# Kernel tuning notes

Measured on AMD Instinct MI355X. Metric: run time of the kernel, lower is better.

## Reference

```python
import jax, jax.numpy as jnp
import numpy as np

N = 8192
EMBED_DIM = 128
TAU = 0.2
MAX_SAMPLES = 10
NEG_INF = -1e9


def setup_inputs() -> dict:
    key = jax.random.key(0)
    k1, k2, k3, k4, k5, k6 = jax.random.split(key, 6)
    user_emb = jax.random.normal(k1, (N, EMBED_DIM), dtype=jnp.float32)
    item_emb = jax.random.normal(k2, (N, EMBED_DIM), dtype=jnp.float32)
    social_edges = jax.random.randint(k3, (2, 131072), 0, N, dtype=jnp.int64)
    # Linear(embed_dim, embed_dim) params
    lim = 1.0 / np.sqrt(EMBED_DIM)
    W = jax.random.uniform(k4, (EMBED_DIM, EMBED_DIM), minval=-lim, maxval=lim, dtype=jnp.float32)
    b = jax.random.uniform(k5, (EMBED_DIM,), minval=-lim, maxval=lim, dtype=jnp.float32)
    # gumbel noise: -log(Exp(1)) == standard Gumbel, matches -empty.exponential_().log()
    gumbel = jax.random.gumbel(k6, (N, N), dtype=jnp.float32)
    return {"user_emb": user_emb, "item_emb": item_emb, "social_edges": social_edges,
            "W": W, "b": b, "gumbel": gumbel}


def reference(user_emb, item_emb, social_edges, W, b, gumbel):
    # projection + similarity
    proj = user_emb @ W.T + b                      # [N, D]
    sim = (proj @ proj.T) / TAU                    # [N, N]
    # mask = eye + scatter of social edges
    mask = jnp.eye(N, dtype=jnp.float32)
    mask = mask.at[social_edges[0], social_edges[1]].set(1.0)
    sim = jnp.where(mask > 0, NEG_INF, sim)
    # gumbel-softmax (soft)
    y_soft = jax.nn.softmax((sim + gumbel) / TAU, axis=-1)
    # top-k scatter -> binary relation matrix
    k = min(MAX_SAMPLES, N - 1)
    _, topk_idx = jax.lax.top_k(y_soft, k)         # [N, k]
    rows = jnp.arange(N)[:, None]
    new_relations = jnp.zeros_like(sim).at[rows, topk_idx].set(1.0)
    return new_relations
```

## Files before the change

### kernel.cpp

```cpp
#include <hip/hip_runtime.h>

#define NROW 8192
#define DIM 128
#define NWORD (NROW / 32)
#define CAP 448
#define MINNORM 1.17549435082228751e-38f

__device__ __attribute__((aligned(16))) float g_Pf[(size_t)NROW * DIM];
__device__ unsigned int g_mask[(size_t)NROW * NWORD];
__device__ float g_ct[(size_t)NROW * CAP];
__device__ int   g_ci[(size_t)NROW * CAP];
__device__ int   g_cnt[NROW];
__device__ unsigned int g_umax[NROW];
__device__ int g_flag;

__device__ __forceinline__ unsigned int umap(float f) {
    unsigned int u = __float_as_uint(f);
    return (u & 0x80000000u) ? ~u : (u | 0x80000000u);
}
__device__ __forceinline__ float finv(unsigned int m) {
    if (m == 0u) return -3.4e38f;
    return (m & 0x80000000u) ? __uint_as_float(m & 0x7FFFFFFFu)
                             : __uint_as_float(~m);
}

__global__ void init_kernel() {
    int i = blockIdx.x * 256 + threadIdx.x;
    if (i < NROW * NWORD) g_mask[i] = 0u;
    if (i < NROW) { g_cnt[i] = 0; g_umax[i] = 0u; }
}

__global__ void detect_i64_kernel(const unsigned int* __restrict__ w) {
    __shared__ unsigned int s;
    if (threadIdx.x == 0) s = 0u;
    __syncthreads();
    unsigned int acc = 0u;
    for (int e = threadIdx.x; e < 4096; e += 256) acc |= w[2 * e + 1];
    atomicOr(&s, acc);
    __syncthreads();
    if (threadIdx.x == 0) g_flag = (s == 0u) ? 1 : 0;
}

__global__ void scatter_edges_kernel(const int* __restrict__ edges, int nedge) {
    int e = blockIdx.x * blockDim.x + threadIdx.x;
    if (e >= nedge) return;
    int r, c;
    if (g_flag) { r = edges[2 * e]; c = edges[2 * (nedge + e)]; }
    else        { r = edges[e];     c = edges[nedge + e]; }
    atomicOr(&g_mask[(size_t)r * NWORD + (c >> 5)], 1u << (c & 31));
}

__global__ void diag_mask_kernel() {
    int i = blockIdx.x * blockDim.x + threadIdx.x;
    atomicOr(&g_mask[(size_t)i * NWORD + (i >> 5)], 1u << (i & 31));
}

__global__ __launch_bounds__(256) void proj_kernel(const float* __restrict__ U,
                                                   const float* __restrict__ W,
                                                   const float* __restrict__ bias) {
    __shared__ float Ws[64][DIM];
    __shared__ float Ur[16][DIM];
    const int tid = threadIdx.x;
    const int i0 = blockIdx.x * 16;
    for (int idx = tid; idx < 16 * DIM; idx += 256)
        ((float*)Ur)[idx] = U[(size_t)i0 * DIM + idx];
    for (int half = 0; half < 2; ++half) {
        __syncthreads();
        for (int idx = tid; idx < 64 * DIM; idx += 256)
            ((float*)Ws)[idx] = W[(size_t)half * 64 * DIM + idx];
        __syncthreads();
        const int d = tid & 63;
        const int rg = tid >> 6;
        const float bb = bias[half * 64 + d];
#pragma unroll
        for (int rr = 0; rr < 4; ++rr) {
            const int row = rg * 4 + rr;
            float a = 0.0f;
#pragma unroll 16
            for (int k = 0; k < DIM; ++k)
                a = fmaf(Ur[row][k], Ws[d][k], a);
            g_Pf[(size_t)(i0 + row) * DIM + half * 64 + d] = a + bb;
        }
    }
}

__global__ __launch_bounds__(256) void scan_kernel(const float* __restrict__ G) {
    __shared__ float rowPT[128][34];
    __shared__ float colS[128][64];
    __shared__ unsigned int umaxl[32];
    __shared__ float thrl[32];
    const int tid = threadIdx.x;
    const int band = blockIdx.x / 3;
    const int chunk = blockIdx.x % 3;
    const int s0 = chunk * 43;
    const int ns = (chunk < 2) ? 43 : 42;
    const int rb = band * 32;
    const int rg2 = (tid >> 4) * 2;
    const int cg4 = (tid & 15) * 4;

    for (int i = tid; i < 32 * 128; i += 256) {
        int r = i >> 7, k = i & 127;
        rowPT[k][r] = g_Pf[(size_t)(rb + r) * DIM + k];
    }
    if (tid < 32) umaxl[tid] = 0u;

    for (int jj = 0; jj <= ns; ++jj) {
        const int j = s0 + (jj ? jj - 1 : 0);
        const bool collect = jj > 0;
        const int c0 = j * 64;
        __syncthreads();
        if (jj != 1) {
            for (int u = tid; u < 64 * 32; u += 256) {
                const int c = u & 63, q = u >> 6;
                const float4 v = *(const float4*)(g_Pf + (size_t)(c0 + c) * DIM + q * 4);
                colS[q * 4 + 0][c] = v.x;
                colS[q * 4 + 1][c] = v.y;
                colS[q * 4 + 2][c] = v.z;
                colS[q * 4 + 3][c] = v.w;
            }
        }
        if (tid < 32) {
            unsigned int mine = umaxl[tid];
            unsigned int old = atomicMax(&g_umax[rb + tid], mine);
            thrl[tid] = fmaxf(finv(old), finv(mine)) - 88.0f;
        }
        __syncthreads();

        float a00 = 0.f, a01 = 0.f, a02 = 0.f, a03 = 0.f;
        float a10 = 0.f, a11 = 0.f, a12 = 0.f, a13 = 0.f;
#pragma unroll 4
        for (int k = 0; k < 128; ++k) {
            const float2 rv = *(const float2*)&rowPT[k][rg2];
            const float4 cv = *(const float4*)&colS[k][cg4];
            a00 = fmaf(rv.x, cv.x, a00); a01 = fmaf(rv.x, cv.y, a01);
            a02 = fmaf(rv.x, cv.z, a02); a03 = fmaf(rv.x, cv.w, a03);
            a10 = fmaf(rv.y, cv.x, a10); a11 = fmaf(rv.y, cv.y, a11);
            a12 = fmaf(rv.y, cv.z, a12); a13 = fmaf(rv.y, cv.w, a13);
        }
#pragma unroll
        for (int r = 0; r < 2; ++r) {
            const int lrow = rg2 + r;
            const int row = rb + lrow;
            const float4 gg = *(const float4*)(G + (size_t)row * NROW + c0 + cg4);
            const unsigned int mw = g_mask[(size_t)row * NWORD + ((c0 + cg4) >> 5)];
            const float thr = thrl[lrow];
            float av[4] = { r ? a10 : a00, r ? a11 : a01, r ? a12 : a02, r ? a13 : a03 };
            float gv[4] = { gg.x, gg.y, gg.z, gg.w };
            float tm = -3.4e38f;
#pragma unroll
            for (int q = 0; q < 4; ++q) {
                const int c = c0 + cg4 + q;
                float s = av[q] / 0.2f;
                if ((mw >> (c & 31)) & 1u) s = -1e9f;
                const float t = (s + gv[q]) / 0.2f;
                tm = fmaxf(tm, t);
                if (collect && t >= thr) {
                    int p = atomicAdd(&g_cnt[row], 1);
                    if (p < CAP) {
                        g_ct[(size_t)row * CAP + p] = t;
                        g_ci[(size_t)row * CAP + p] = c;
                    }
                }
            }
            atomicMax(&umaxl[lrow], umap(tm));
        }
    }
}

__global__ __launch_bounds__(256) void finalize_kernel(float* __restrict__ out) {
    __shared__ float es[NROW];
    __shared__ float redf[256];
    __shared__ float pwA[64], pwB[32];
    __shared__ unsigned long long rull[256];
    __shared__ unsigned long long plv[512];
    __shared__ unsigned int bmp[NROW / 32];
    __shared__ int wl[10];
    __shared__ unsigned int wyb[10];
    __shared__ int npos;
    const int tid = threadIdx.x;
    const int row = blockIdx.x;

    int cnt = g_cnt[row]; if (cnt > CAP) cnt = CAP;

    float m = -3.4e38f;
    for (int i = tid; i < cnt; i += 256) m = fmaxf(m, g_ct[(size_t)row * CAP + i]);
    redf[tid] = m;
    if (tid == 0) npos = 0;
    for (int i = tid; i < NROW / 4; i += 256) ((float4*)es)[i] = float4{0.f, 0.f, 0.f, 0.f};
    if (tid < NWORD) bmp[tid] = 0u;
    __syncthreads();
    for (int s = 128; s; s >>= 1) { if (tid < s) redf[tid] = fmaxf(redf[tid], redf[tid + s]); __syncthreads(); }
    const float tmax = redf[0];
    __syncthreads();

    for (int i = tid; i < cnt; i += 256) {
        const float t = g_ct[(size_t)row * CAP + i];
        const int pos = g_ci[(size_t)row * CAP + i];
        const float d = t - tmax;
        float e = 0.0f;
        if (d >= -87.4f) {
            e = (float)exp((double)d);
            if (e < MINNORM) e = 0.0f;
        }
        es[pos] = e;
    }
    __syncthreads();

    if (tid < 64) {
        const float* x = &es[tid * 128];
        float r0 = x[0], r1 = x[1], r2 = x[2], r3 = x[3];
        float r4 = x[4], r5 = x[5], r6 = x[6], r7 = x[7];
        for (int i = 8; i < 128; i += 8) {
            r0 += x[i + 0]; r1 += x[i + 1]; r2 += x[i + 2]; r3 += x[i + 3];
            r4 += x[i + 4]; r5 += x[i + 5]; r6 += x[i + 6]; r7 += x[i + 7];
        }
        pwA[tid] = ((r0 + r1) + (r2 + r3)) + ((r4 + r5) + (r6 + r7));
    }
    __syncthreads();
    if (tid < 32) pwB[tid] = pwA[2 * tid] + pwA[2 * tid + 1];
    __syncthreads();
    if (tid < 16) pwA[tid] = pwB[2 * tid] + pwB[2 * tid + 1];
    __syncthreads();
    if (tid < 8) pwB[tid] = pwA[2 * tid] + pwA[2 * tid + 1];
    __syncthreads();
    if (tid < 4) pwA[tid] = pwB[2 * tid] + pwB[2 * tid + 1];
    __syncthreads();
    if (tid < 2) pwB[tid] = pwA[2 * tid] + pwA[2 * tid + 1];
    __syncthreads();
    if (tid == 0) pwA[0] = pwB[0] + pwB[1];
    __syncthreads();
    const float Sf = pwA[0];

    for (int i = tid; i < cnt; i += 256) {
        const int pos = g_ci[(size_t)row * CAP + i];
        float yv = es[pos] / Sf;
        if (yv < MINNORM) yv = 0.0f;
        if (yv > 0.0f) {
            int sl = atomicAdd(&npos, 1);
            plv[sl] = ((unsigned long long)__float_as_uint(yv) << 32) |
                      (unsigned int)(NROW - 1 - pos);
            atomicOr(&bmp[pos >> 5], 1u << (pos & 31));
        }
    }
    __syncthreads();
    const int np = npos;

    for (int it = 0; it < 10; ++it) {
        unsigned long long best = 0ull;
        for (int i = tid; i < np; i += 256) best = best > plv[i] ? best : plv[i];
        rull[tid] = best;
        __syncthreads();
        for (int s = 128; s; s >>= 1) {
            if (tid < s && rull[tid + s] > rull[tid]) rull[tid] = rull[tid + s];
            __syncthreads();
        }
        const unsigned long long wb = rull[0];
        __syncthreads();
        if (tid == 0) {
            if (wb) { wl[it] = NROW - 1 - (int)(wb & 0xFFFFFFFFu); wyb[it] = (unsigned int)(wb >> 32); }
            else    { wl[it] = -1; wyb[it] = 0u; }
        }
        if (wb) for (int i = tid; i < np; i += 256) if (plv[i] == wb) plv[i] = 0ull;
        __syncthreads();
    }

    if (tid == 0) {
        int pos = 0;
        for (int it = 0; it < 10; ++it) {
            if (wl[it] >= 0) continue;
            while ((bmp[pos >> 5] >> (pos & 31)) & 1u) ++pos;
            wl[it] = pos; wyb[it] = 0u; ++pos;
        }
    }
    __syncthreads();

    for (int i = tid; i < NROW; i += 256) es[i] = 0.0f;
    __syncthreads();
    if (tid < 10) {
        float v;
        if (wyb[tid] == 0u)              v = 1.015625f;
        else if (wyb[tid] < 0x01800000u) v = 1.0078125f;
        else                             v = 1.0f;
        es[wl[tid]] = v;
    }
    __syncthreads();
    for (int i = tid; i < NROW / 4; i += 256)
        ((float4*)(out + (size_t)row * NROW))[i] = ((const float4*)es)[i];
}

extern "C" void kernel_launch(void* const* d_in, const int* in_sizes, int n_in,
                              void* d_out, int out_size, void* d_ws, size_t ws_size,
                              hipStream_t stream) {
    const float* U = (const float*)d_in[0];
    const int* edges = (const int*)d_in[2];
    const float* W = (const float*)d_in[3];
    const float* bias = (const float*)d_in[4];
    const float* G = (const float*)d_in[5];
    const int nedge = in_sizes[2] / 2;
    float* out = (float*)d_out;

    init_kernel<<<(NROW * NWORD + 255) / 256, 256, 0, stream>>>();
    detect_i64_kernel<<<1, 256, 0, stream>>>((const unsigned int*)edges);
    scatter_edges_kernel<<<(nedge + 255) / 256, 256, 0, stream>>>(edges, nedge);
    diag_mask_kernel<<<NROW / 256, 256, 0, stream>>>();
    proj_kernel<<<NROW / 16, 256, 0, stream>>>(U, W, bias);
    scan_kernel<<<256 * 3, 256, 0, stream>>>(G);
    finalize_kernel<<<NROW, 256, 0, stream>>>(out);
}
```

Baseline: 749.5 us.

## Use bf16 MFMA scan with candidate filtering and exact fp32 recompute in finalize

The similarity scan now runs on bf16 MFMA (16x16x32) with per-wave 16-row tiles and a per-lane running max, and it keeps only the column indices within a wide window of that max. The finalize kernel recomputes the exact fp32 dot products, mask and Gumbel terms for those candidates in shared memory. This is meant to replace the scalar fp32 shared-memory GEMM and the global atomicMax threshold exchange with matrix-core throughput. The trade-offs are bf16 rounding in the filter, which the wide window and exact recompute are meant to absorb, a larger candidate capacity, and more uncoalesced Gumbel and projection reads in finalize.

```diff
diff --git a/kernel.cpp b/kernel.cpp
--- a/kernel.cpp
+++ b/kernel.cpp
@@ -3,31 +3,29 @@
 #define NROW 8192
 #define DIM 128
 #define NWORD (NROW / 32)
-#define CAP 448
+#define CAP 1024
 #define MINNORM 1.17549435082228751e-38f
+#define WINDOW 100.0f
+#define WAVES 8
+#define ROWS_PB 16
+#define COLS_PER_STEP (WAVES * 16)
+#define NSTEP (NROW / COLS_PER_STEP)
+#define WARM 4
+
+typedef __attribute__((ext_vector_type(8))) short bf16x8;
+typedef __attribute__((ext_vector_type(4))) float f32x4;
 
 __device__ __attribute__((aligned(16))) float g_Pf[(size_t)NROW * DIM];
+__device__ __attribute__((aligned(16))) unsigned short g_Pbf[(size_t)NROW * DIM];
 __device__ unsigned int g_mask[(size_t)NROW * NWORD];
-__device__ float g_ct[(size_t)NROW * CAP];
-__device__ int   g_ci[(size_t)NROW * CAP];
-__device__ int   g_cnt[NROW];
-__device__ unsigned int g_umax[NROW];
+__device__ int g_ci[(size_t)NROW * CAP];
+__device__ int g_cnt[NROW];
 __device__ int g_flag;
-
-__device__ __forceinline__ unsigned int umap(float f) {
-    unsigned int u = __float_as_uint(f);
-    return (u & 0x80000000u) ? ~u : (u | 0x80000000u);
-}
-__device__ __forceinline__ float finv(unsigned int m) {
-    if (m == 0u) return -3.4e38f;
-    return (m & 0x80000000u) ? __uint_as_float(m & 0x7FFFFFFFu)
-                             : __uint_as_float(~m);
-}
 
 __global__ void init_kernel() {
     int i = blockIdx.x * 256 + threadIdx.x;
     if (i < NROW * NWORD) g_mask[i] = 0u;
-    if (i < NROW) { g_cnt[i] = 0; g_umax[i] = 0u; }
+    if (i < NROW) g_cnt[i] = 0;
 }
 
 __global__ void detect_i64_kernel(const unsigned int* __restrict__ w) {
@@ -79,101 +77,86 @@
 #pragma unroll 16
             for (int k = 0; k < DIM; ++k)
                 a = fmaf(Ur[row][k], Ws[d][k], a);
-            g_Pf[(size_t)(i0 + row) * DIM + half * 64 + d] = a + bb;
-        }
-    }
-}
-
-__global__ __launch_bounds__(256) void scan_kernel(const float* __restrict__ G) {
-    __shared__ float rowPT[128][34];
-    __shared__ float colS[128][64];
-    __shared__ unsigned int umaxl[32];
-    __shared__ float thrl[32];
+            const float pj = a + bb;
+            const size_t off = (size_t)(i0 + row) * DIM + half * 64 + d;
+            g_Pf[off] = pj;
+            unsigned int u = __float_as_uint(pj);
+            g_Pbf[off] = (unsigned short)((u + 0x7fffu + ((u >> 16) & 1u)) >> 16);
+        }
+    }
+}
+
+__global__ __launch_bounds__(512) void scan_kernel(const float* __restrict__ G) {
     const int tid = threadIdx.x;
-    const int band = blockIdx.x / 3;
-    const int chunk = blockIdx.x % 3;
-    const int s0 = chunk * 43;
-    const int ns = (chunk < 2) ? 43 : 42;
-    const int rb = band * 32;
-    const int rg2 = (tid >> 4) * 2;
-    const int cg4 = (tid & 15) * 4;
-
-    for (int i = tid; i < 32 * 128; i += 256) {
-        int r = i >> 7, k = i & 127;
-        rowPT[k][r] = g_Pf[(size_t)(rb + r) * DIM + k];
-    }
-    if (tid < 32) umaxl[tid] = 0u;
-
-    for (int jj = 0; jj <= ns; ++jj) {
-        const int j = s0 + (jj ? jj - 1 : 0);
-        const bool collect = jj > 0;
-        const int c0 = j * 64;
-        __syncthreads();
-        if (jj != 1) {
-            for (int u = tid; u < 64 * 32; u += 256) {
-                const int c = u & 63, q = u >> 6;
-                const float4 v = *(const float4*)(g_Pf + (size_t)(c0 + c) * DIM + q * 4);
-                colS[q * 4 + 0][c] = v.x;
-                colS[q * 4 + 1][c] = v.y;
-                colS[q * 4 + 2][c] = v.z;
-                colS[q * 4 + 3][c] = v.w;
-            }
-        }
-        if (tid < 32) {
-            unsigned int mine = umaxl[tid];
-            unsigned int old = atomicMax(&g_umax[rb + tid], mine);
-            thrl[tid] = fmaxf(finv(old), finv(mine)) - 88.0f;
-        }
-        __syncthreads();
-
-        float a00 = 0.f, a01 = 0.f, a02 = 0.f, a03 = 0.f;
-        float a10 = 0.f, a11 = 0.f, a12 = 0.f, a13 = 0.f;
-#pragma unroll 4
-        for (int k = 0; k < 128; ++k) {
-            const float2 rv = *(const float2*)&rowPT[k][rg2];
-            const float4 cv = *(const float4*)&colS[k][cg4];
-            a00 = fmaf(rv.x, cv.x, a00); a01 = fmaf(rv.x, cv.y, a01);
-            a02 = fmaf(rv.x, cv.z, a02); a03 = fmaf(rv.x, cv.w, a03);
-            a10 = fmaf(rv.y, cv.x, a10); a11 = fmaf(rv.y, cv.y, a11);
-            a12 = fmaf(rv.y, cv.z, a12); a13 = fmaf(rv.y, cv.w, a13);
-        }
-#pragma unroll
-        for (int r = 0; r < 2; ++r) {
-            const int lrow = rg2 + r;
-            const int row = rb + lrow;
-            const float4 gg = *(const float4*)(G + (size_t)row * NROW + c0 + cg4);
-            const unsigned int mw = g_mask[(size_t)row * NWORD + ((c0 + cg4) >> 5)];
-            const float thr = thrl[lrow];
-            float av[4] = { r ? a10 : a00, r ? a11 : a01, r ? a12 : a02, r ? a13 : a03 };
-            float gv[4] = { gg.x, gg.y, gg.z, gg.w };
-            float tm = -3.4e38f;
-#pragma unroll
-            for (int q = 0; q < 4; ++q) {
-                const int c = c0 + cg4 + q;
-                float s = av[q] / 0.2f;
-                if ((mw >> (c & 31)) & 1u) s = -1e9f;
-                const float t = (s + gv[q]) / 0.2f;
-                tm = fmaxf(tm, t);
-                if (collect && t >= thr) {
-                    int p = atomicAdd(&g_cnt[row], 1);
-                    if (p < CAP) {
-                        g_ct[(size_t)row * CAP + p] = t;
-                        g_ci[(size_t)row * CAP + p] = c;
-                    }
+    const int lane = tid & 63;
+    const int wv = tid >> 6;
+    const int rb = blockIdx.x * ROWS_PB;
+    const int l15 = lane & 15;
+    const int lg = lane >> 4;
+
+    bf16x8 Bf[4];
+#pragma unroll
+    for (int kf = 0; kf < 4; ++kf)
+        Bf[kf] = *(const bf16x8*)(g_Pbf + (size_t)(rb + l15) * DIM + kf * 32 + lg * 8);
+
+    const int myrow = rb + l15;
+    const unsigned int* mrow = g_mask + (size_t)myrow * NWORD;
+    const float* grow = G + (size_t)myrow * NROW;
+    float rmax = -3.4e38f;
+
+    for (int it = 0; it < NSTEP + WARM; ++it) {
+        const int step = (it < WARM) ? it : it - WARM;
+        const bool collect = it >= WARM;
+        const int cb = step * COLS_PER_STEP + wv * 16;
+
+        bf16x8 Af[4];
+#pragma unroll
+        for (int kf = 0; kf < 4; ++kf)
+            Af[kf] = *(const bf16x8*)(g_Pbf + (size_t)(cb + l15) * DIM + kf * 32 + lg * 8);
+        f32x4 acc = {0.f, 0.f, 0.f, 0.f};
+#pragma unroll
+        for (int kf = 0; kf < 4; ++kf)
+            acc = __builtin_amdgcn_mfma_f32_16x16x32_bf16(Af[kf], Bf[kf], acc, 0, 0, 0);
+
+        const int c0 = cb + lg * 4;
+        const float4 gg = *(const float4*)(grow + c0);
+        const unsigned int mw = mrow[c0 >> 5];
+        const float thr = rmax - WINDOW;
+        float z[4];
+        float zm = -3.4e38f;
+#pragma unroll
+        for (int j = 0; j < 4; ++j) {
+            const bool msk = (mw >> ((c0 + j) & 31)) & 1u;
+            const float gj = j == 0 ? gg.x : (j == 1 ? gg.y : (j == 2 ? gg.z : gg.w));
+            z[j] = msk ? -3.0e38f : fmaf(acc[j], 25.0f, gj * 5.0f);
+            zm = fmaxf(zm, z[j]);
+        }
+        if (collect) {
+#pragma unroll
+            for (int j = 0; j < 4; ++j) {
+                if (z[j] >= thr) {
+                    int p = atomicAdd(&g_cnt[myrow], 1);
+                    if (p < CAP) g_ci[(size_t)myrow * CAP + p] = c0 + j;
                 }
             }
-            atomicMax(&umaxl[lrow], umap(tm));
-        }
-    }
-}
-
-__global__ __launch_bounds__(256) void finalize_kernel(float* __restrict__ out) {
+        }
+        zm = fmaxf(zm, __shfl_xor(zm, 16));
+        zm = fmaxf(zm, __shfl_xor(zm, 32));
+        rmax = fmaxf(rmax, zm);
+    }
+}
+
+__global__ __launch_bounds__(256) void finalize_kernel(const float* __restrict__ G,
+                                                       float* __restrict__ out) {
     __shared__ float es[NROW];
+    __shared__ float prow[DIM];
+    __shared__ float ct[CAP];
+    __shared__ int ci[CAP];
     __shared__ float redf[256];
     __shared__ float pwA[64], pwB[32];
     __shared__ unsigned long long rull[256];
-    __shared__ unsigned long long plv[512];
-    __shared__ unsigned int bmp[NROW / 32];
+    __shared__ unsigned long long plv[CAP];
+    __shared__ unsigned int bmp[NWORD];
     __shared__ int wl[10];
     __shared__ unsigned int wyb[10];
     __shared__ int npos;
@@ -181,28 +164,48 @@
     const int row = blockIdx.x;
 
     int cnt = g_cnt[row]; if (cnt > CAP) cnt = CAP;
+    if (tid < DIM) prow[tid] = g_Pf[(size_t)row * DIM + tid];
+    if (tid == 0) npos = 0;
+    if (tid < NWORD) bmp[tid] = 0u;
+    for (int i = tid; i < NROW / 4; i += 256) ((float4*)es)[i] = float4{0.f, 0.f, 0.f, 0.f};
+    __syncthreads();
+
+    for (int i = tid; i < cnt; i += 256) {
+        const int c = g_ci[(size_t)row * CAP + i];
+        const float4* pc = (const float4*)(g_Pf + (size_t)c * DIM);
+        float a = 0.0f;
+#pragma unroll 8
+        for (int q = 0; q < 32; ++q) {
+            const float4 v = pc[q];
+            const float4 pr = *(const float4*)&prow[q * 4];
+            a = fmaf(pr.x, v.x, a);
+            a = fmaf(pr.y, v.y, a);
+            a = fmaf(pr.z, v.z, a);
+            a = fmaf(pr.w, v.w, a);
+        }
+        float s = a / 0.2f;
+        if ((g_mask[(size_t)row * NWORD + (c >> 5)] >> (c & 31)) & 1u) s = -1e9f;
+        const float t = (s + G[(size_t)row * NROW + c]) / 0.2f;
+        ct[i] = t; ci[i] = c;
+    }
+    __syncthreads();
 
     float m = -3.4e38f;
-    for (int i = tid; i < cnt; i += 256) m = fmaxf(m, g_ct[(size_t)row * CAP + i]);
+    for (int i = tid; i < cnt; i += 256) m = fmaxf(m, ct[i]);
     redf[tid] = m;
-    if (tid == 0) npos = 0;
-    for (int i = tid; i < NROW / 4; i += 256) ((float4*)es)[i] = float4{0.f, 0.f, 0.f, 0.f};
-    if (tid < NWORD) bmp[tid] = 0u;
     __syncthreads();
     for (int s = 128; s; s >>= 1) { if (tid < s) redf[tid] = fmaxf(redf[tid], redf[tid + s]); __syncthreads(); }
     const float tmax = redf[0];
     __syncthreads();
 
     for (int i = tid; i < cnt; i += 256) {
-        const float t = g_ct[(size_t)row * CAP + i];
-        const int pos = g_ci[(size_t)row * CAP + i];
-        const float d = t - tmax;
+        const float d = ct[i] - tmax;
         float e = 0.0f;
         if (d >= -87.4f) {
             e = (float)exp((double)d);
             if (e < MINNORM) e = 0.0f;
         }
-        es[pos] = e;
+        es[ci[i]] = e;
     }
     __syncthreads();
 
@@ -232,7 +235,7 @@
     const float Sf = pwA[0];
 
     for (int i = tid; i < cnt; i += 256) {
-        const int pos = g_ci[(size_t)row * CAP + i];
+        const int pos = ci[i];
         float yv = es[pos] / Sf;
         if (yv < MINNORM) yv = 0.0f;
         if (yv > 0.0f) {
@@ -304,6 +307,6 @@
     scatter_edges_kernel<<<(nedge + 255) / 256, 256, 0, stream>>>(edges, nedge);
     diag_mask_kernel<<<NROW / 256, 256, 0, stream>>>();
     proj_kernel<<<NROW / 16, 256, 0, stream>>>(U, W, bias);
-    scan_kernel<<<256 * 3, 256, 0, stream>>>(G);
-    finalize_kernel<<<NROW, 256, 0, stream>>>(out);
-}
+    scan_kernel<<<NROW / ROWS_PB, 512, 0, stream>>>(G);
+    finalize_kernel<<<NROW, 256, 0, stream>>>(G, out);
+}
```

New measurement: 691.9 us. -7.7%, faster.
